# Performance work log

Hardware: AMD Instinct MI355X
Metric: run time of the kernel (lower is better)

Reference implementation:

```python
import jax, jax.numpy as jnp
import numpy as np

B, S, IN, HID, H, D, FF = 8, 2048, 512, 512, 8, 64, 2048
EPS = 1e-5


def layer_norm(x, g, b):
    m = jnp.mean(x, axis=-1, keepdims=True)
    v = jnp.mean(jnp.square(x - m), axis=-1, keepdims=True)
    return (x - m) * jax.lax.rsqrt(v + EPS) * g + b


def delta_rule(q, k, v, beta):
    # q,k,v: [S,B,H,D]; beta: [S,B,H,1]
    # W_t = W_{t-1} + beta_t*(v_t - W_{t-1} k_t) k_t^T ; out_t = W_t q_t
    def step(W, inp):
        qt, kt, vt, bt = inp
        wk = jnp.einsum('bhde,bhe->bhd', W, kt)
        v_new = bt * (vt - wk)
        W = W + jnp.einsum('bhd,bhe->bhde', v_new, kt)
        out = jnp.einsum('bhde,bhe->bhd', W, qt)
        return W, out

    bsz = q.shape[1]
    W0 = jnp.zeros((bsz, H, D, D), dtype=q.dtype)
    _, outs = jax.lax.scan(step, W0, (q, k, v, beta))
    return outs  # [S,B,H,D]


def fast_ff(x, ln_g, ln_b, slow_w, out_w):
    # x: [S,B,HID]
    slen, bsz, _ = x.shape
    h = layer_norm(x, ln_g, ln_b)
    qkvb = jnp.einsum('sbi,oi->sbo', h, slow_w).reshape(slen, bsz, H, 3 * D + 1)
    q, k, v, beta = jnp.split(qkvb, [D, 2 * D, 3 * D], axis=-1)
    q = jax.nn.softmax(q, axis=-1)
    k = jax.nn.softmax(k, axis=-1)
    beta = jax.nn.sigmoid(beta)
    attn = delta_rule(q, k, v, beta)  # [S,B,H,D]
    o = jnp.einsum('sbd,od->sbo', attn.reshape(slen, bsz, H * D), out_w)
    return x + o


def ffn(x, ln_g, ln_b, w1, b1, w2, b2):
    h = layer_norm(x, ln_g, ln_b)
    h = jax.nn.relu(jnp.einsum('sbi,fi->sbf', h, w1) + b1)
    return x + jnp.einsum('sbf,of->sbo', h, w2) + b2


def setup_inputs() -> dict:
    key = jax.random.key(0)
    ks = jax.random.split(key, 8)
    s = 0.02
    return {
        'x': jax.random.normal(ks[0], (B, S, IN), jnp.float32),
        'ip_w': s * jax.random.normal(ks[1], (HID, IN), jnp.float32),
        'ip_b': jnp.zeros((HID,), jnp.float32),
        'fw_ln_g': jnp.ones((2, HID), jnp.float32),
        'fw_ln_b': jnp.zeros((2, HID), jnp.float32),
        'fw_slow_w': s * jax.random.normal(ks[2], (2, H * (3 * D + 1), HID), jnp.float32),
        'fw_out_w': s * jax.random.normal(ks[3], (2, HID, H * D), jnp.float32),
        'ff_ln_g': jnp.ones((HID,), jnp.float32),
        'ff_ln_b': jnp.zeros((HID,), jnp.float32),
        'ff_w1': s * jax.random.normal(ks[4], (FF, HID), jnp.float32),
        'ff_b1': jnp.zeros((FF,), jnp.float32),
        'ff_w2': s * jax.random.normal(ks[5], (HID, FF), jnp.float32),
        'ff_b2': jnp.zeros((HID,), jnp.float32),
    }


def reference(x, ip_w, ip_b, fw_ln_g, fw_ln_b, fw_slow_w, fw_out_w,
              ff_ln_g, ff_ln_b, ff_w1, ff_b1, ff_w2, ff_b2):
    out = jnp.einsum('bsi,hi->bsh', x, ip_w) + ip_b  # input_proj
    out = out.transpose(1, 0, 2)  # [S,B,HID]
    out = fast_ff(out, fw_ln_g[0], fw_ln_b[0], fw_slow_w[0], fw_out_w[0])
    out = ffn(out, ff_ln_g, ff_ln_b, ff_w1, ff_b1, ff_w2, ff_b2)
    out = fast_ff(out, fw_ln_g[1], fw_ln_b[1], fw_slow_w[1], fw_out_w[1])
    return out.transpose(1, 0, 2)  # [B,S,HID]
```

## Files before the change

kernel.cpp:

```cpp
#include <hip/hip_runtime.h>
#include <hip/hip_bf16.h>

#define B_    8
#define S_    2048
#define HID_  512
#define H_    8
#define D_    64
#define FF_   2048
#define QN_   1664
#define NCH_  32
#define SLOWSTRIDE (1544 * 512)

typedef unsigned short u16;
typedef __attribute__((ext_vector_type(8))) short short8;
typedef __attribute__((ext_vector_type(4))) float f32x4;

__device__ __forceinline__ u16 f2bf(float x) {
  unsigned u = __builtin_bit_cast(unsigned, x);
  unsigned r = (u + 0x7FFFu + ((u >> 16) & 1u)) >> 16;
  return (u16)r;
}
__device__ __forceinline__ float bf2f(u16 v) {
  return __builtin_bit_cast(float, (unsigned)v << 16);
}
__device__ __forceinline__ void gload16(const void* g, void* l) {
  __builtin_amdgcn_global_load_lds(
      (const __attribute__((address_space(1))) unsigned int*)g,
      (__attribute__((address_space(3))) unsigned int*)l, 16, 0, 0);
}

template<int FS, int GS>
__device__ __forceinline__ void prod64(const u16* __restrict__ F,
                                       const u16* __restrict__ G,
                                       int wrow0, int lane, f32x4 acc[4])
{
  short8 f0 = *(const short8*)&F[(wrow0 + (lane & 15)) * FS + ((lane >> 4) * 8)];
  short8 f1 = *(const short8*)&F[(wrow0 + (lane & 15)) * FS + 32 + ((lane >> 4) * 8)];
  #pragma unroll
  for (int c0 = 0; c0 < 4; ++c0) {
    short8 g0 = *(const short8*)&G[(c0 * 16 + (lane & 15)) * GS + ((lane >> 4) * 8)];
    short8 g1 = *(const short8*)&G[(c0 * 16 + (lane & 15)) * GS + 32 + ((lane >> 4) * 8)];
    acc[c0] = __builtin_amdgcn_mfma_f32_16x16x32_bf16(f0, g0, acc[c0], 0, 0, 0);
    acc[c0] = __builtin_amdgcn_mfma_f32_16x16x32_bf16(f1, g1, acc[c0], 0, 0, 0);
  }
}

template<bool BIAS, bool RELU, bool RES, bool OUTBF, bool TRANS, bool QKVB>
__global__ __launch_bounds__(256, 4) void gemm_bf(
    const u16* __restrict__ A, const u16* __restrict__ W,
    const float* __restrict__ bias, const float* __restrict__ res,
    void* __restrict__ Cout, int M, int N, int K)
{
  __shared__ __align__(16) u16 SH[16384];
  const int tid = threadIdx.x, lane = tid & 63, wv = tid >> 6;
  const int bm = blockIdx.y * 128, bn = blockIdx.x * 128;
  const int wr = wv >> 1, wc = wv & 1;
  const int row16 = lane & 15, kg = lane >> 4;
  const int srow = lane >> 2;
  const int ssoff = ((lane & 3) ^ (srow & 3)) * 16;

  f32x4 acc[4][4] = {};
  const int ktiles = K >> 5;

  auto STAGE = [&](int buf, int kt) {
    u16* As = &SH[buf * 8192];
    u16* Bs = &SH[buf * 8192 + 4096];
    #pragma unroll
    for (int i = 0; i < 2; ++i) {
      const int r = i * 64 + wv * 16;
      const char* ga = (const char*)(A + (size_t)(bm + r + srow) * K + (size_t)kt * 32) + ssoff;
      gload16(ga, &As[r * 32]);
      const char* gw = (const char*)(W + (size_t)(bn + r + srow) * K + (size_t)kt * 32) + ssoff;
      gload16(gw, &Bs[r * 32]);
    }
  };

  STAGE(0, 0);
  __syncthreads();
  int buf = 0;
  for (int kt = 0; kt < ktiles; ++kt) {
    if (kt + 1 < ktiles) STAGE(buf ^ 1, kt + 1);
    const u16* As = &SH[buf * 8192];
    const u16* Bs = &SH[buf * 8192 + 4096];
    short8 af[4], bf_[4];
    #pragma unroll
    for (int m = 0; m < 4; ++m) {
      const int lrow = wr * 64 + m * 16 + row16;
      af[m] = *(const short8*)&As[lrow * 32 + (kg ^ (lrow & 3)) * 8];
    }
    #pragma unroll
    for (int n = 0; n < 4; ++n) {
      const int lrow = wc * 64 + n * 16 + row16;
      bf_[n] = *(const short8*)&Bs[lrow * 32 + (kg ^ (lrow & 3)) * 8];
    }
    #pragma unroll
    for (int m = 0; m < 4; ++m)
      #pragma unroll
      for (int n = 0; n < 4; ++n)
        acc[m][n] = __builtin_amdgcn_mfma_f32_16x16x32_bf16(af[m], bf_[n], acc[m][n], 0, 0, 0);
    __syncthreads();
    buf ^= 1;
  }

  if (QKVB) {
    const int span0 = bn + wc * 64;
    #pragma unroll
    for (int m = 0; m < 4; ++m) {
      #pragma unroll
      for (int j = 0; j < 4; ++j) {
        if (span0 < 1024) {
          float v0 = acc[m][0][j], v1 = acc[m][1][j];
          float v2 = acc[m][2][j], v3 = acc[m][3][j];
          float mx = fmaxf(fmaxf(v0, v1), fmaxf(v2, v3));
          #pragma unroll
          for (int off = 1; off < 16; off <<= 1) mx = fmaxf(mx, __shfl_xor(mx, off));
          float e0 = __expf(v0 - mx), e1 = __expf(v1 - mx);
          float e2 = __expf(v2 - mx), e3 = __expf(v3 - mx);
          float s = (e0 + e1) + (e2 + e3);
          #pragma unroll
          for (int off = 1; off < 16; off <<= 1) s += __shfl_xor(s, off);
          float r = 1.f / s;
          acc[m][0][j] = e0 * r; acc[m][1][j] = e1 * r;
          acc[m][2][j] = e2 * r; acc[m][3][j] = e3 * r;
        } else if (span0 >= 1536) {
          #pragma unroll
          for (int n = 0; n < 4; ++n)
            acc[m][n][j] = 1.f / (1.f + __expf(-acc[m][n][j]));
        }
      }
    }
  }

  float* LD = (float*)SH;
  #pragma unroll
  for (int p = 0; p < 4; ++p) {
    if (p) __syncthreads();
    if (wr == (p >> 1)) {
      #pragma unroll
      for (int mm = 0; mm < 2; ++mm) {
        const int m = (p & 1) * 2 + mm;
        #pragma unroll
        for (int n = 0; n < 4; ++n)
          #pragma unroll
          for (int j = 0; j < 4; ++j)
            LD[(mm * 16 + kg * 4 + j) * 132 + wc * 64 + n * 16 + row16] = acc[m][n][j];
      }
    }
    __syncthreads();
    #pragma unroll
    for (int step = 0; step < 4; ++step) {
      int linear = step * 256 + tid;
      int row = linear >> 5, q = linear & 31;
      float4 v = *(const float4*)&LD[row * 132 + q * 4];
      const int grow = bm + p * 32 + row;
      const int gcol = bn + q * 4;
      if (BIAS) {
        float4 b4 = *(const float4*)&bias[gcol];
        v.x += b4.x; v.y += b4.y; v.z += b4.z; v.w += b4.w;
      }
      if (RES) {
        float4 r4 = *(const float4*)&res[(size_t)grow * N + gcol];
        v.x += r4.x; v.y += r4.y; v.z += r4.z; v.w += r4.w;
      }
      if (RELU) {
        v.x = fmaxf(v.x, 0.f); v.y = fmaxf(v.y, 0.f);
        v.z = fmaxf(v.z, 0.f); v.w = fmaxf(v.w, 0.f);
      }
      size_t gr = TRANS ? ((size_t)(grow & 7) * S_ + (grow >> 3)) : (size_t)grow;
      if (OUTBF) {
        uint2 pk;
        pk.x = (unsigned)f2bf(v.x) | ((unsigned)f2bf(v.y) << 16);
        pk.y = (unsigned)f2bf(v.z) | ((unsigned)f2bf(v.w) << 16);
        *(uint2*)&((u16*)Cout)[gr * N + gcol] = pk;
      } else {
        *(float4*)&((float*)Cout)[gr * N + gcol] = v;
      }
    }
  }
}

__global__ __launch_bounds__(256) void conv_w(const float* __restrict__ s,
                                              u16* __restrict__ d, int n, int npad)
{
  int i = blockIdx.x * 256 + threadIdx.x;
  if (i < npad) d[i] = (i < n) ? f2bf(s[i]) : (u16)0;
}

__global__ __launch_bounds__(256) void conv_slow(const float* __restrict__ s,
                                                 u16* __restrict__ d)
{
  int r = blockIdx.x;
  int src;
  if (r < 512)       src = (r >> 6) * 193 + (r & 63);
  else if (r < 1024) src = ((r - 512) >> 6) * 193 + 64 + (r & 63);
  else if (r < 1536) src = ((r - 1024) >> 6) * 193 + 128 + (r & 63);
  else if (r < 1544) src = (r - 1536) * 193 + 192;
  else               src = -1;
  for (int c = threadIdx.x; c < 512; c += 256)
    d[(size_t)r * 512 + c] = (src >= 0) ? f2bf(s[(size_t)src * 512 + c]) : (u16)0;
}

__global__ __launch_bounds__(64) void conv_x(const float* __restrict__ x,
                                             u16* __restrict__ xbf)
{
  size_t m = blockIdx.x;
  size_t s = m >> 3, b = m & 7;
  const float4* src = (const float4*)(x + (b * (size_t)S_ + s) * HID_);
  float4 v0 = src[threadIdx.x], v1 = src[64 + threadIdx.x];
  u16* dst = xbf + m * HID_;
  uint2 p0, p1;
  p0.x = (unsigned)f2bf(v0.x) | ((unsigned)f2bf(v0.y) << 16);
  p0.y = (unsigned)f2bf(v0.z) | ((unsigned)f2bf(v0.w) << 16);
  p1.x = (unsigned)f2bf(v1.x) | ((unsigned)f2bf(v1.y) << 16);
  p1.y = (unsigned)f2bf(v1.z) | ((unsigned)f2bf(v1.w) << 16);
  *(uint2*)&dst[threadIdx.x * 4] = p0;
  *(uint2*)&dst[256 + threadIdx.x * 4] = p1;
}

__global__ __launch_bounds__(64) void ln_bf(const float* __restrict__ x,
    const float* __restrict__ g, const float* __restrict__ bt,
    u16* __restrict__ o)
{
  size_t row = blockIdx.x;
  int lane = threadIdx.x;
  const float4* xr = (const float4*)(x + row * HID_);
  float4 v0 = xr[lane];
  float4 v1 = xr[64 + lane];
  float s  = v0.x + v0.y + v0.z + v0.w + v1.x + v1.y + v1.z + v1.w;
  float ss = v0.x*v0.x + v0.y*v0.y + v0.z*v0.z + v0.w*v0.w
           + v1.x*v1.x + v1.y*v1.y + v1.z*v1.z + v1.w*v1.w;
  #pragma unroll
  for (int off = 32; off; off >>= 1) {
    s  += __shfl_xor(s, off);
    ss += __shfl_xor(ss, off);
  }
  float mean = s * (1.f / HID_);
  float inv  = rsqrtf(ss * (1.f / HID_) - mean * mean + 1e-5f);
  const float4* gv = (const float4*)g;
  const float4* bv = (const float4*)bt;
  float4 g0 = gv[lane], g1 = gv[64 + lane];
  float4 b0 = bv[lane], b1 = bv[64 + lane];
  uint2 p0, p1;
  p0.x = (unsigned)f2bf((v0.x - mean) * inv * g0.x + b0.x)
       | ((unsigned)f2bf((v0.y - mean) * inv * g0.y + b0.y) << 16);
  p0.y = (unsigned)f2bf((v0.z - mean) * inv * g0.z + b0.z)
       | ((unsigned)f2bf((v0.w - mean) * inv * g0.w + b0.w) << 16);
  p1.x = (unsigned)f2bf((v1.x - mean) * inv * g1.x + b1.x)
       | ((unsigned)f2bf((v1.y - mean) * inv * g1.y + b1.y) << 16);
  p1.y = (unsigned)f2bf((v1.z - mean) * inv * g1.z + b1.z)
       | ((unsigned)f2bf((v1.w - mean) * inv * g1.w + b1.w) << 16);
  u16* ov = o + row * HID_;
  *(uint2*)&ov[lane * 4] = p0;
  *(uint2*)&ov[256 + lane * 4] = p1;
}

__global__ __launch_bounds__(256, 2) void delta_p1(const u16* __restrict__ qf,
                                                   u16* __restrict__ MTg,
                                                   u16* __restrict__ Ng,
                                                   u16* __restrict__ CKg,
                                                   u16* __restrict__ U0Tg)
{
  __shared__ __align__(16) u16 Kb[64 * 72];
  __shared__ __align__(16) float Am[64][65];
  __shared__ __align__(16) float Uv[64][65];
  __shared__ __align__(16) float Uk[64][65];
  __shared__ __align__(16) u16 CKTb[64 * 72];
  __shared__ __align__(16) u16 U0Tb[64 * 72];
  __shared__ float bet[64];
  u16* KTb = (u16*)&Am[0][0];

  const int id5 = blockIdx.x, bh = id5 >> 5;
  const int b = bh & 7, h = bh >> 3, t0 = (id5 & 31) * 64;
  const int tid = threadIdx.x, lane = tid & 63, wv = tid >> 6;
  const int wid = wv, wrow0 = wv * 16;

  #pragma unroll
  for (int p = 0; p < 2; ++p) {
    int linear = p * 256 + tid, row = linear >> 3, seg = linear & 7;
    uint4 k4 = *(const uint4*)&qf[((size_t)(t0 + row) * B_ + b) * QN_ + 512 + h * 64 + seg * 8];
    *(short8*)&Kb[row * 72 + seg * 8] = __builtin_bit_cast(short8, k4);
  }
  if (tid < 64) bet[tid] = bf2f(qf[((size_t)(t0 + tid) * B_ + b) * QN_ + 1536 + h]);
  __syncthreads();

  {
    f32x4 a[4] = {};
    prod64<72, 72>(Kb, Kb, wrow0, lane, a);
    #pragma unroll
    for (int c0 = 0; c0 < 4; ++c0)
      #pragma unroll
      for (int j = 0; j < 4; ++j) {
        int row = wrow0 + (lane >> 4) * 4 + j, col = c0 * 16 + (lane & 15);
        Am[row][col] = bet[row] * a[c0][j];
      }
  }
  #pragma unroll
  for (int p = 0; p < 2; ++p) {
    int linear = p * 256 + tid, row = linear >> 3, seg = linear & 7;
    float bt_ = bet[row];
    uint4 v4 = *(const uint4*)&qf[((size_t)(t0 + row) * B_ + b) * QN_ + 1024 + h * 64 + seg * 8];
    short8 vs = __builtin_bit_cast(short8, v4);
    short8 ks = *(const short8*)&Kb[row * 72 + seg * 8];
    #pragma unroll
    for (int e = 0; e < 8; ++e) {
      Uv[row][seg * 8 + e] = bt_ * bf2f((u16)vs[e]);
      Uk[row][seg * 8 + e] = bt_ * bf2f((u16)ks[e]);
    }
  }
  __syncthreads();

  #pragma unroll 1
  for (int blk = 0; blk < 4; ++blk) {
    if (wid == blk) {
      const int r0 = blk * 16;
      float uv[16], uk[16];
      #pragma unroll
      for (int i = 0; i < 16; ++i) { uv[i] = Uv[r0 + i][lane]; uk[i] = Uk[r0 + i][lane]; }
      #pragma unroll
      for (int jj = 0; jj < 15; ++jj) {
        #pragma unroll
        for (int t = jj + 1; t < 16; ++t) {
          float a = Am[r0 + t][r0 + jj];
          uv[t] = fmaf(-a, uv[jj], uv[t]);
          uk[t] = fmaf(-a, uk[jj], uk[t]);
        }
      }
      #pragma unroll
      for (int i = 0; i < 16; ++i) { Uv[r0 + i][lane] = uv[i]; Uk[r0 + i][lane] = uk[i]; }
    }
    __syncthreads();
    if (wid > blk) {
      const int r0 = blk * 16, rw = wid * 16;
      float uv[16], uk[16];
      #pragma unroll
      for (int i = 0; i < 16; ++i) { uv[i] = Uv[rw + i][lane]; uk[i] = Uk[rw + i][lane]; }
      #pragma unroll
      for (int jj = 0; jj < 16; ++jj) {
        float sv = Uv[r0 + jj][lane], sk = Uk[r0 + jj][lane];
        #pragma unroll
        for (int i = 0; i < 16; ++i) {
          float a = Am[rw + i][r0 + jj];
          uv[i] = fmaf(-a, sv, uv[i]);
          uk[i] = fmaf(-a, sk, uk[i]);
        }
      }
      #pragma unroll
      for (int i = 0; i < 16; ++i) { Uv[rw + i][lane] = uv[i]; Uk[rw + i][lane] = uk[i]; }
    }
    __syncthreads();
  }

  const int prow = tid >> 2, pc0 = (tid & 3) * 16;
  const size_t mb = (size_t)id5 * 4096;
  {
    union { u16 u[16]; uint4 v[2]; } pk, pu;
    #pragma unroll
    for (int i = 0; i < 16; ++i) pk.u[i] = f2bf(Uk[prow][pc0 + i]);
    #pragma unroll
    for (int i = 0; i < 16; ++i) pu.u[i] = f2bf(Uv[pc0 + i][prow]);
    *(uint4*)&CKg[mb + prow * 64 + pc0]      = pk.v[0];
    *(uint4*)&CKg[mb + prow * 64 + pc0 + 8]  = pk.v[1];
    *(uint4*)&U0Tg[mb + prow * 64 + pc0]     = pu.v[0];
    *(uint4*)&U0Tg[mb + prow * 64 + pc0 + 8] = pu.v[1];
    *(short8*)&U0Tb[prow * 72 + pc0]     = *(short8*)&pu.u[0];
    *(short8*)&U0Tb[prow * 72 + pc0 + 8] = *(short8*)&pu.u[8];
    #pragma unroll
    for (int i = 0; i < 16; ++i) CKTb[prow * 72 + pc0 + i] = f2bf(Uk[pc0 + i][prow]);
    #pragma unroll
    for (int i = 0; i < 16; ++i) KTb[prow * 88 + pc0 + i] = Kb[(pc0 + i) * 72 + prow];
  }
  __syncthreads();

  {
    f32x4 am[4] = {}, an[4] = {};
    prod64<88, 72>(KTb, CKTb, wrow0, lane, am);
    prod64<72, 88>(U0Tb, KTb, wrow0, lane, an);
    #pragma unroll
    for (int c0 = 0; c0 < 4; ++c0)
      #pragma unroll
      for (int j = 0; j < 4; ++j) {
        int row = wrow0 + (lane >> 4) * 4 + j, col = c0 * 16 + (lane & 15);
        MTg[mb + (size_t)row * 64 + col] = f2bf(am[c0][j]);
        Ng[mb + (size_t)row * 64 + col]  = f2bf(an[c0][j]);
      }
  }
}

__global__ __launch_bounds__(256, 1) void delta_p2(const u16* __restrict__ MTg,
                                                   const u16* __restrict__ Ng,
                                                   u16* __restrict__ Wsnap)
{
  __shared__ float Ws[64][65];
  __shared__ __align__(16) u16 Wbf[64 * 72];
  __shared__ __align__(16) u16 MTb[64 * 72];
  __shared__ __align__(16) u16 Nb[64 * 72];
  const int bh = blockIdx.x;
  const int tid = threadIdx.x, lane = tid & 63, wv = tid >> 6, wrow0 = wv * 16;
  const int prow = tid >> 2, pc0 = (tid & 3) * 16;

  for (int i = tid; i < 64 * 65; i += 256) (&Ws[0][0])[i] = 0.f;
  for (int i = tid; i < 64 * 72; i += 256) Wbf[i] = 0;
  __syncthreads();

  size_t base = (size_t)bh * NCH_ * 4096;
  uint4 rm0 = *(const uint4*)&MTg[base + prow * 64 + pc0];
  uint4 rm1 = *(const uint4*)&MTg[base + prow * 64 + pc0 + 8];
  uint4 rn0 = *(const uint4*)&Ng[base + prow * 64 + pc0];
  uint4 rn1 = *(const uint4*)&Ng[base + prow * 64 + pc0 + 8];

  for (int j = 0; j < NCH_; ++j) {
    *(short8*)&MTb[prow * 72 + pc0]     = __builtin_bit_cast(short8, rm0);
    *(short8*)&MTb[prow * 72 + pc0 + 8] = __builtin_bit_cast(short8, rm1);
    *(short8*)&Nb[prow * 72 + pc0]      = __builtin_bit_cast(short8, rn0);
    *(short8*)&Nb[prow * 72 + pc0 + 8]  = __builtin_bit_cast(short8, rn1);
    {
      size_t sb = base + (size_t)j * 4096;
      short8 w0 = *(const short8*)&Wbf[prow * 72 + pc0];
      short8 w1 = *(const short8*)&Wbf[prow * 72 + pc0 + 8];
      *(uint4*)&Wsnap[sb + prow * 64 + pc0]     = __builtin_bit_cast(uint4, w0);
      *(uint4*)&Wsnap[sb + prow * 64 + pc0 + 8] = __builtin_bit_cast(uint4, w1);
    }
    if (j + 1 < NCH_) {
      size_t nb2 = base + (size_t)(j + 1) * 4096;
      rm0 = *(const uint4*)&MTg[nb2 + prow * 64 + pc0];
      rm1 = *(const uint4*)&MTg[nb2 + prow * 64 + pc0 + 8];
      rn0 = *(const uint4*)&Ng[nb2 + prow * 64 + pc0];
      rn1 = *(const uint4*)&Ng[nb2 + prow * 64 + pc0 + 8];
    }
    __syncthreads();
    f32x4 a[4] = {};
    prod64<72, 72>(Wbf, MTb, wrow0, lane, a);
    #pragma unroll
    for (int c0 = 0; c0 < 4; ++c0)
      #pragma unroll
      for (int jj = 0; jj < 4; ++jj) {
        int row = wrow0 + (lane >> 4) * 4 + jj, col = c0 * 16 + (lane & 15);
        float w = Ws[row][col] + bf2f(Nb[row * 72 + col]) - a[c0][jj];
        Ws[row][col] = w;
        Wbf[row * 72 + col] = f2bf(w);
      }
    __syncthreads();
  }
}

__global__ __launch_bounds__(256, 2) void delta_p3(const u16* __restrict__ qf,
                                                   const u16* __restrict__ Wsnap,
                                                   const u16* __restrict__ CKg,
                                                   const u16* __restrict__ U0Tg,
                                                   u16* __restrict__ attnb)
{
  __shared__ __align__(16) u16 Qb[64 * 72];
  __shared__ __align__(16) u16 Kb[64 * 72];
  __shared__ __align__(16) u16 W0b[64 * 72];
  __shared__ __align__(16) u16 CKb[64 * 72];
  __shared__ __align__(16) u16 U0Tb[64 * 72];
  __shared__ __align__(16) u16 Gb[64 * 72];
  __shared__ __align__(16) u16 UTb[64 * 72];

  const int id5 = blockIdx.x, bh = id5 >> 5;
  const int b = bh & 7, h = bh >> 3, t0 = (id5 & 31) * 64;
  const int tid = threadIdx.x, lane = tid & 63, wv = tid >> 6, wrow0 = wv * 16;
  const int prow = tid >> 2, pc0 = (tid & 3) * 16;
  const size_t mb = (size_t)id5 * 4096;

  #pragma unroll
  for (int p = 0; p < 2; ++p) {
    int linear = p * 256 + tid, row = linear >> 3, seg = linear & 7;
    size_t gb = ((size_t)(t0 + row) * B_ + b) * QN_;
    uint4 q4 = *(const uint4*)&qf[gb + h * 64 + seg * 8];
    uint4 k4 = *(const uint4*)&qf[gb + 512 + h * 64 + seg * 8];
    uint4 w4 = *(const uint4*)&Wsnap[mb + (size_t)row * 64 + seg * 8];
    *(short8*)&Qb[row * 72 + seg * 8]  = __builtin_bit_cast(short8, q4);
    *(short8*)&Kb[row * 72 + seg * 8]  = __builtin_bit_cast(short8, k4);
    *(short8*)&W0b[row * 72 + seg * 8] = __builtin_bit_cast(short8, w4);
  }
  {
    uint4 c0v = *(const uint4*)&CKg[mb + prow * 64 + pc0];
    uint4 c1v = *(const uint4*)&CKg[mb + prow * 64 + pc0 + 8];
    uint4 u0v = *(const uint4*)&U0Tg[mb + prow * 64 + pc0];
    uint4 u1v = *(const uint4*)&U0Tg[mb + prow * 64 + pc0 + 8];
    *(short8*)&CKb[prow * 72 + pc0]      = __builtin_bit_cast(short8, c0v);
    *(short8*)&CKb[prow * 72 + pc0 + 8]  = __builtin_bit_cast(short8, c1v);
    *(short8*)&U0Tb[prow * 72 + pc0]     = __builtin_bit_cast(short8, u0v);
    *(short8*)&U0Tb[prow * 72 + pc0 + 8] = __builtin_bit_cast(short8, u1v);
  }
  __syncthreads();

  f32x4 ag[4] = {}, ac[4] = {}, ab[4] = {};
  prod64<72, 72>(Qb, Kb, wrow0, lane, ag);
  prod64<72, 72>(W0b, CKb, wrow0, lane, ac);
  prod64<72, 72>(Qb, W0b, wrow0, lane, ab);

  #pragma unroll
  for (int c0 = 0; c0 < 4; ++c0)
    #pragma unroll
    for (int j = 0; j < 4; ++j) {
      int row = wrow0 + (lane >> 4) * 4 + j, col = c0 * 16 + (lane & 15);
      Gb[row * 72 + col]  = f2bf(col <= row ? ag[c0][j] : 0.f);
      UTb[row * 72 + col] = f2bf(bf2f(U0Tb[row * 72 + col]) - ac[c0][j]);
    }
  __syncthreads();

  prod64<72, 72>(Gb, UTb, wrow0, lane, ab);

  #pragma unroll
  for (int c0 = 0; c0 < 4; ++c0)
    #pragma unroll
    for (int j = 0; j < 4; ++j) {
      int row = wrow0 + (lane >> 4) * 4 + j, col = c0 * 16 + (lane & 15);
      attnb[((size_t)(t0 + row) * B_ + b) * HID_ + h * 64 + col] = f2bf(ab[c0][j]);
    }
}

extern "C" void kernel_launch(void* const* d_in, const int* in_sizes, int n_in,
                              void* d_out, int out_size, void* d_ws, size_t ws_size,
                              hipStream_t stream)
{
  const float* x        = (const float*)d_in[0];
  const float* ip_w     = (const float*)d_in[1];
  const float* ip_b     = (const float*)d_in[2];
  const float* fw_ln_g  = (const float*)d_in[3];
  const float* fw_ln_b  = (const float*)d_in[4];
  const float* fw_slow_w = (const float*)d_in[5];
  const float* fw_out_w  = (const float*)d_in[6];
  const float* ff_ln_g  = (const float*)d_in[7];
  const float* ff_ln_b  = (const float*)d_in[8];
  const float* ff_w1    = (const float*)d_in[9];
  const float* ff_b1    = (const float*)d_in[10];
  const float* ff_w2    = (const float*)d_in[11];
  const float* ff_b2    = (const float*)d_in[12];
  float* out = (float*)d_out;

  const int M = B_ * S_;
  const size_t matN = (size_t)64 * NCH_ * 4096;

  const size_t nIp = 512 * 512, nOut = 512 * 512;
  const size_t nSlow = (size_t)QN_ * 512;
  const size_t nW1 = (size_t)FF_ * 512, nW2 = (size_t)512 * FF_;
  const size_t nXbf = (size_t)M * HID_;
  const size_t poolElems = nIp + 2 * nSlow + 2 * nOut + nW1 + nW2 + nXbf + matN;

  size_t need = (size_t)M * HID_ * 4
              + ((size_t)M * QN_ + 2 * matN + poolElems) * 2;
  if (ws_size < need) return;

  float* cur   = (float*)d_ws;
  u16*   qkvbf = (u16*)(cur + (size_t)M * HID_);
  u16*   attnSlot = qkvbf + (size_t)M * QN_;
  u16*   MTg   = attnSlot;
  u16*   Ng    = MTg + matN;
  u16*   attnb = attnSlot;
  u16*   CKg   = (u16*)out;
  u16*   U0Tg  = CKg + matN;
  u16*   tmpbf = (u16*)out;
  u16*   hiddenb = qkvbf;

  u16* pool = attnSlot + 2 * matN;
  u16* ipwb   = pool;               pool += nIp;
  u16* slowb0 = pool;               pool += nSlow;
  u16* slowb1 = pool;               pool += nSlow;
  u16* outwb0 = pool;               pool += nOut;
  u16* outwb1 = pool;               pool += nOut;
  u16* w1b    = pool;               pool += nW1;
  u16* w2b    = pool;               pool += nW2;
  u16* Wsnap  = pool;               pool += matN;
  u16* xbf    = pool;

  dim3 blk(256);

  conv_w<<<(nIp + 255) / 256, blk, 0, stream>>>(ip_w, ipwb, nIp, nIp);
  conv_slow<<<QN_, blk, 0, stream>>>(fw_slow_w, slowb0);
  conv_slow<<<QN_, blk, 0, stream>>>(fw_slow_w + (size_t)SLOWSTRIDE, slowb1);
  conv_w<<<(nOut + 255) / 256, blk, 0, stream>>>(fw_out_w, outwb0, nOut, nOut);
  conv_w<<<(nOut + 255) / 256, blk, 0, stream>>>(fw_out_w + (size_t)512 * 512, outwb1, nOut, nOut);
  conv_w<<<(nW1 + 255) / 256, blk, 0, stream>>>(ff_w1, w1b, nW1, nW1);
  conv_w<<<(nW2 + 255) / 256, blk, 0, stream>>>(ff_w2, w2b, nW2, nW2);
  conv_x<<<M, 64, 0, stream>>>(x, xbf);

  gemm_bf<true, false, false, false, false, false><<<dim3(4, 128), blk, 0, stream>>>(
      xbf, ipwb, ip_b, nullptr, cur, M, HID_, HID_);

  for (int layer = 0; layer < 2; ++layer) {
    u16* slowb = layer ? slowb1 : slowb0;
    u16* outwb = layer ? outwb1 : outwb0;

    ln_bf<<<M, 64, 0, stream>>>(cur, fw_ln_g + layer * HID_, fw_ln_b + layer * HID_, tmpbf);
    gemm_bf<false, false, false, true, false, true><<<dim3(13, 128), blk, 0, stream>>>(
        tmpbf, slowb, nullptr, nullptr, qkvbf, M, QN_, HID_);
    delta_p1<<<64 * NCH_, 256, 0, stream>>>(qkvbf, MTg, Ng, CKg, U0Tg);
    delta_p2<<<64, 256, 0, stream>>>(MTg, Ng, Wsnap);
    delta_p3<<<64 * NCH_, 256, 0, stream>>>(qkvbf, Wsnap, CKg, U0Tg, attnb);
    if (layer == 0) {
      gemm_bf<false, false, true, false, false, false><<<dim3(4, 128), blk, 0, stream>>>(
          attnb, outwb, nullptr, cur, cur, M, HID_, HID_);
      ln_bf<<<M, 64, 0, stream>>>(cur, ff_ln_g, ff_ln_b, tmpbf);
      gemm_bf<true, true, false, true, false, false><<<dim3(16, 128), blk, 0, stream>>>(
          tmpbf, w1b, ff_b1, nullptr, hiddenb, M, FF_, HID_);
      gemm_bf<true, false, true, false, false, false><<<dim3(4, 128), blk, 0, stream>>>(
          hiddenb, w2b, ff_b2, cur, cur, M, HID_, FF_);
    } else {
      gemm_bf<false, false, true, false, true, false><<<dim3(4, 128), blk, 0, stream>>>(
          attnb, outwb, nullptr, cur, out, M, HID_, HID_);
    }
  }
}
```

Measured before the change: 556.5 us.

## Shrink delta_p1 shared memory with bf16 staging and register-resident U rows

Replaces the three fp32 64x65 shared arrays in the chunk-local triangular solve with bf16 buffers: a bf16 beta*KK^T matrix reused later as K^T, and small 16-row staging buffers for the solved block. Each wave now keeps its 16 rows of Uv/Uk in registers for the whole forward substitution instead of reloading and storing them every block step. Launch bounds are raised to 3 blocks per CU. The cut in LDS traffic and footprint is meant to raise occupancy, at the cost of rounding A and intermediate U values to bf16 and a narrower store pattern for CKg.

New measurement: 543.9 us. 2.3% less time.

```diff
diff --git a/kernel.cpp b/kernel.cpp
--- a/kernel.cpp
+++ b/kernel.cpp
@@ -254,25 +254,25 @@
   *(uint2*)&ov[256 + lane * 4] = p1;
 }
 
-__global__ __launch_bounds__(256, 2) void delta_p1(const u16* __restrict__ qf,
+__global__ __launch_bounds__(256, 3) void delta_p1(const u16* __restrict__ qf,
                                                    u16* __restrict__ MTg,
                                                    u16* __restrict__ Ng,
                                                    u16* __restrict__ CKg,
                                                    u16* __restrict__ U0Tg)
 {
   __shared__ __align__(16) u16 Kb[64 * 72];
-  __shared__ __align__(16) float Am[64][65];
-  __shared__ __align__(16) float Uv[64][65];
-  __shared__ __align__(16) float Uk[64][65];
+  __shared__ __align__(16) u16 AmKT[64 * 72];
+  __shared__ __align__(16) u16 stV[16 * 72];
+  __shared__ __align__(16) u16 stK[16 * 72];
   __shared__ __align__(16) u16 CKTb[64 * 72];
   __shared__ __align__(16) u16 U0Tb[64 * 72];
   __shared__ float bet[64];
-  u16* KTb = (u16*)&Am[0][0];
 
   const int id5 = blockIdx.x, bh = id5 >> 5;
   const int b = bh & 7, h = bh >> 3, t0 = (id5 & 31) * 64;
   const int tid = threadIdx.x, lane = tid & 63, wv = tid >> 6;
   const int wid = wv, wrow0 = wv * 16;
+  const size_t mb = (size_t)id5 * 4096;
 
   #pragma unroll
   for (int p = 0; p < 2; ++p) {
@@ -291,21 +291,17 @@
       #pragma unroll
       for (int j = 0; j < 4; ++j) {
         int row = wrow0 + (lane >> 4) * 4 + j, col = c0 * 16 + (lane & 15);
-        Am[row][col] = bet[row] * a[c0][j];
-      }
-  }
-  #pragma unroll
-  for (int p = 0; p < 2; ++p) {
-    int linear = p * 256 + tid, row = linear >> 3, seg = linear & 7;
-    float bt_ = bet[row];
-    uint4 v4 = *(const uint4*)&qf[((size_t)(t0 + row) * B_ + b) * QN_ + 1024 + h * 64 + seg * 8];
-    short8 vs = __builtin_bit_cast(short8, v4);
-    short8 ks = *(const short8*)&Kb[row * 72 + seg * 8];
-    #pragma unroll
-    for (int e = 0; e < 8; ++e) {
-      Uv[row][seg * 8 + e] = bt_ * bf2f((u16)vs[e]);
-      Uk[row][seg * 8 + e] = bt_ * bf2f((u16)ks[e]);
-    }
+        AmKT[row * 72 + col] = f2bf(bet[row] * a[c0][j]);
+      }
+  }
+
+  float uv[16], uk[16];
+  #pragma unroll
+  for (int i = 0; i < 16; ++i) {
+    const int row = wrow0 + i;
+    const float bt_ = bet[row];
+    uv[i] = bt_ * bf2f(qf[((size_t)(t0 + row) * B_ + b) * QN_ + 1024 + h * 64 + lane]);
+    uk[i] = bt_ * bf2f(Kb[row * 72 + lane]);
   }
   __syncthreads();
 
@@ -313,68 +309,59 @@
   for (int blk = 0; blk < 4; ++blk) {
     if (wid == blk) {
       const int r0 = blk * 16;
-      float uv[16], uk[16];
-      #pragma unroll
-      for (int i = 0; i < 16; ++i) { uv[i] = Uv[r0 + i][lane]; uk[i] = Uk[r0 + i][lane]; }
       #pragma unroll
       for (int jj = 0; jj < 15; ++jj) {
         #pragma unroll
         for (int t = jj + 1; t < 16; ++t) {
-          float a = Am[r0 + t][r0 + jj];
+          float a = bf2f(AmKT[(r0 + t) * 72 + r0 + jj]);
           uv[t] = fmaf(-a, uv[jj], uv[t]);
           uk[t] = fmaf(-a, uk[jj], uk[t]);
         }
       }
       #pragma unroll
-      for (int i = 0; i < 16; ++i) { Uv[r0 + i][lane] = uv[i]; Uk[r0 + i][lane] = uk[i]; }
+      for (int i = 0; i < 16; ++i) {
+        stV[i * 72 + lane] = f2bf(uv[i]);
+        stK[i * 72 + lane] = f2bf(uk[i]);
+      }
     }
     __syncthreads();
     if (wid > blk) {
-      const int r0 = blk * 16, rw = wid * 16;
-      float uv[16], uk[16];
-      #pragma unroll
-      for (int i = 0; i < 16; ++i) { uv[i] = Uv[rw + i][lane]; uk[i] = Uk[rw + i][lane]; }
+      const int r0 = blk * 16;
       #pragma unroll
       for (int jj = 0; jj < 16; ++jj) {
-        float sv = Uv[r0 + jj][lane], sk = Uk[r0 + jj][lane];
+        float sv = bf2f(stV[jj * 72 + lane]);
+        float sk = bf2f(stK[jj * 72 + lane]);
         #pragma unroll
         for (int i = 0; i < 16; ++i) {
-          float a = Am[rw + i][r0 + jj];
+          float a = bf2f(AmKT[(wrow0 + i) * 72 + r0 + jj]);
           uv[i] = fmaf(-a, sv, uv[i]);
           uk[i] = fmaf(-a, sk, uk[i]);
         }
       }
-      #pragma unroll
-      for (int i = 0; i < 16; ++i) { Uv[rw + i][lane] = uv[i]; Uk[rw + i][lane] = uk[i]; }
     }
     __syncthreads();
   }
 
-  const int prow = tid >> 2, pc0 = (tid & 3) * 16;
-  const size_t mb = (size_t)id5 * 4096;
+  #pragma unroll
+  for (int i = 0; i < 16; ++i) {
+    const int row = wrow0 + i;
+    u16 ck = f2bf(uk[i]), u0 = f2bf(uv[i]);
+    CKg[mb + (size_t)row * 64 + lane] = ck;
+    CKTb[lane * 72 + row] = ck;
+    U0Tb[lane * 72 + row] = u0;
+  }
   {
-    union { u16 u[16]; uint4 v[2]; } pk, pu;
-    #pragma unroll
-    for (int i = 0; i < 16; ++i) pk.u[i] = f2bf(Uk[prow][pc0 + i]);
-    #pragma unroll
-    for (int i = 0; i < 16; ++i) pu.u[i] = f2bf(Uv[pc0 + i][prow]);
-    *(uint4*)&CKg[mb + prow * 64 + pc0]      = pk.v[0];
-    *(uint4*)&CKg[mb + prow * 64 + pc0 + 8]  = pk.v[1];
-    *(uint4*)&U0Tg[mb + prow * 64 + pc0]     = pu.v[0];
-    *(uint4*)&U0Tg[mb + prow * 64 + pc0 + 8] = pu.v[1];
-    *(short8*)&U0Tb[prow * 72 + pc0]     = *(short8*)&pu.u[0];
-    *(short8*)&U0Tb[prow * 72 + pc0 + 8] = *(short8*)&pu.u[8];
-    #pragma unroll
-    for (int i = 0; i < 16; ++i) CKTb[prow * 72 + pc0 + i] = f2bf(Uk[pc0 + i][prow]);
-    #pragma unroll
-    for (int i = 0; i < 16; ++i) KTb[prow * 88 + pc0 + i] = Kb[(pc0 + i) * 72 + prow];
+    const int prow = tid >> 2, pc0 = (tid & 3) * 16;
+    #pragma unroll
+    for (int i = 0; i < 16; ++i)
+      AmKT[prow * 72 + pc0 + i] = Kb[(pc0 + i) * 72 + prow];
   }
   __syncthreads();
 
   {
     f32x4 am[4] = {}, an[4] = {};
-    prod64<88, 72>(KTb, CKTb, wrow0, lane, am);
-    prod64<72, 88>(U0Tb, KTb, wrow0, lane, an);
+    prod64<72, 72>(AmKT, CKTb, wrow0, lane, am);
+    prod64<72, 72>(U0Tb, AmKT, wrow0, lane, an);
     #pragma unroll
     for (int c0 = 0; c0 < 4; ++c0)
       #pragma unroll
@@ -383,6 +370,11 @@
         MTg[mb + (size_t)row * 64 + col] = f2bf(am[c0][j]);
         Ng[mb + (size_t)row * 64 + col]  = f2bf(an[c0][j]);
       }
+    const int prow = tid >> 2, pc0 = (tid & 3) * 16;
+    short8 a0 = *(const short8*)&U0Tb[prow * 72 + pc0];
+    short8 a1 = *(const short8*)&U0Tb[prow * 72 + pc0 + 8];
+    *(uint4*)&U0Tg[mb + prow * 64 + pc0]     = __builtin_bit_cast(uint4, a0);
+    *(uint4*)&U0Tg[mb + prow * 64 + pc0 + 8] = __builtin_bit_cast(uint4, a1);
   }
 }
 
```
